# Performance work log

Hardware: AMD Instinct MI355X
Metric: run time of the kernel (lower is better)

Reference implementation:

```python
import jax, jax.numpy as jnp
import numpy as np

Q, B, N, DIM, HEADS, CODES = 4, 8, 4096, 1024, 8, 1024
DH = DIM // HEADS  # codebook_dim = 128
SCALE = DH ** -0.5


def setup_inputs() -> dict:
    key = jax.random.key(0)
    k0, k1, k2, k3 = jax.random.split(key, 4)
    return {
        "x": jax.random.normal(k0, (B, N, DIM), jnp.float32),
        "codes": jax.random.normal(k1, (Q, HEADS, CODES, DH), jnp.float32),
        "wk": jax.random.normal(k2, (Q, HEADS, DH, DH), jnp.float32) * SCALE,
        "wv": jax.random.normal(k3, (Q, HEADS, DH, DH), jnp.float32) * SCALE,
    }


def _memcodes_layer(x, codes, wk, wv):
    """One Memcodes quantizer (eval path: hard argmax).
    x: [B,N,DIM]; codes: [H,C,DH]; wk/wv: [H,DH,DH].
    Returns quantized [B,N,DIM], indices [B,H,N]."""
    b, n, _ = x.shape
    q = x.reshape(b, n, HEADS, DH).transpose(0, 2, 1, 3) * SCALE  # [b,h,n,d]
    k = jnp.einsum('hnd,hdc->hnc', codes, wk)  # [h,C,d]
    v = jnp.einsum('hnd,hdc->hnc', codes, wv)  # [h,C,d]
    logits = jnp.einsum('bhid,hjd->bhij', q, k)  # [b,h,n,C]
    idx = jnp.argmax(logits, axis=-1)  # [b,h,n]
    # one_hot(idx) @ v == gather rows of v at idx
    out = jnp.take_along_axis(v[None], idx[..., None], axis=2)  # [b,h,n,d]
    out = out.transpose(0, 2, 1, 3).reshape(b, n, DIM)
    return out, idx


def reference(x, codes, wk, wv):
    residual = x
    quantized_out = jnp.zeros_like(x)
    all_indices = []
    for i in range(Q):  # fixed small loop over quantizer layers
        quantized, idx = _memcodes_layer(residual, codes[i], wk[i], wv[i])
        residual = residual - quantized
        quantized_out = quantized_out + quantized
        all_indices.append(idx)
    return quantized_out, jnp.stack(all_indices, axis=-1)  # [B,N,DIM], [B,H,N,Q]
```

## Files before the change

kernel.cpp:

```cpp
#include <hip/hip_runtime.h>
#include <math.h>

#define QL 4
#define BB 8
#define NN 4096
#define DIMF 1024
#define HH 8
#define CC 1024
#define DH 128

#define MARGIN 4e-3f

typedef __attribute__((ext_vector_type(4))) float f32x4;
typedef __attribute__((ext_vector_type(8))) short s16x8;

__device__ __forceinline__ unsigned short f2bf(float f) {
    unsigned int u = __float_as_uint(f);
    u = u + 0x7fffu + ((u >> 16) & 1u);
    return (unsigned short)(u >> 16);
}
__device__ __forceinline__ float bf2f(unsigned short b) {
    return __uint_as_float(((unsigned int)b) << 16);
}
__device__ __forceinline__ void dma16(const void* g, void* l) {
    __builtin_amdgcn_global_load_lds(
        (const __attribute__((address_space(1))) unsigned int*)g,
        (__attribute__((address_space(3))) unsigned int*)l, 16, 0, 0);
}

#define MFMA(a, bb, c) c = __builtin_amdgcn_mfma_f32_16x16x32_bf16(a, bb, c, 0, 0, 0)

__device__ __forceinline__ void upd(float& m1, float& m2, int& mi, float v, int c) {
    if (v > m1) { m2 = m1; m1 = v; mi = c; }
    else if (v > m2) m2 = v;
}

__global__ __launch_bounds__(128) void kv_kernel(
    const float* __restrict__ codes, const float* __restrict__ wk,
    const float* __restrict__ wv, unsigned short* __restrict__ khi,
    unsigned short* __restrict__ klo, float* __restrict__ vbuf)
{
    __shared__ float sc[8][128];
    int bid = blockIdx.x;
    int cg  = bid & 127;
    int qh  = bid >> 7;
    int t   = threadIdx.x;

    const float* cbase = codes + ((size_t)qh * CC + (size_t)cg * 8) * DH;
    #pragma unroll
    for (int i = 0; i < 8; ++i) sc[i][t] = cbase[i * DH + t];
    __syncthreads();

    const float* wkb = wk + (size_t)qh * DH * DH;
    const float* wvb = wv + (size_t)qh * DH * DH;

    float ak[8], av[8];
    #pragma unroll
    for (int i = 0; i < 8; ++i) { ak[i] = 0.f; av[i] = 0.f; }

    for (int d = 0; d < DH; ++d) {
        float a = wkb[d * DH + t];
        float b = wvb[d * DH + t];
        #pragma unroll
        for (int i = 0; i < 8; ++i) {
            ak[i] = fmaf(sc[i][d], a, ak[i]);
            av[i] = fmaf(sc[i][d], b, av[i]);
        }
    }

    size_t base = ((size_t)qh * CC + (size_t)cg * 8) * DH + t;
    #pragma unroll
    for (int i = 0; i < 8; ++i) {
        float f = ak[i];
        unsigned short hb = f2bf(f);
        unsigned short lb = f2bf(f - bf2f(hb));
        khi[base + (size_t)i * DH]  = hb;
        klo[base + (size_t)i * DH]  = lb;
        vbuf[base + (size_t)i * DH] = av[i];
    }
}

__global__ __launch_bounds__(256, 2) void fused_kernel(
    const float* __restrict__ x, const unsigned short* __restrict__ khi,
    const unsigned short* __restrict__ klo, const float* __restrict__ vbuf,
    const float* __restrict__ codes, const float* __restrict__ wk,
    const float* __restrict__ wv, float* __restrict__ out)
{
    __shared__ __align__(16) char kstage[2][32768];
    __shared__ int    chosen[128];
    __shared__ float  smax1[128];
    __shared__ int    flagged[128];
    __shared__ int    hist[QL][128];
    __shared__ int    nflag;
    __shared__ float  rbuf32[DH];
    __shared__ double rbuf64[DH];
    __shared__ double pbuf[DH];
    __shared__ int    cand[64];
    __shared__ int    ncand;
    __shared__ int    bestc;
    __shared__ double bestv;

    const int t  = threadIdx.x;
    const int w  = t >> 6;
    const int l  = t & 63;
    const int lr = l & 15;
    const int lg = l >> 4;

    const int bid = blockIdx.x;
    const int h   = bid & 7;
    const int nt  = (bid >> 3) & 31;
    const int b   = bid >> 8;
    const int n0  = nt * 128;

    const int colE  = ((l & 15) << 4) ^ ((l >> 4) << 4) ^ (((l >> 3) & 1) << 5);
    const int loffE = ((l >> 4) << 8) + colE;
    const int loffO = loffE ^ 0x40;

    s16x8 rhi[2][4], rlo[2][4];
    #pragma unroll
    for (int s = 0; s < 2; ++s) {
        const int tok = (s * 4 + w) * 16 + lr;
        const float* xp = x + ((size_t)(b * NN + n0 + tok)) * DIMF + h * DH;
        #pragma unroll
        for (int ks = 0; ks < 4; ++ks) {
            const float* p = xp + ks * 32 + lg * 8;
            float4 a = *reinterpret_cast<const float4*>(p);
            float4 c = *reinterpret_cast<const float4*>(p + 4);
            float vv[8] = {a.x, a.y, a.z, a.w, c.x, c.y, c.z, c.w};
            s16x8 hi8, lo8;
            #pragma unroll
            for (int j = 0; j < 8; ++j) {
                unsigned short hb = f2bf(vv[j]);
                unsigned short lb = f2bf(vv[j] - bf2f(hb));
                hi8[j] = (short)hb; lo8[j] = (short)lb;
            }
            rhi[s][ks] = hi8; rlo[s][ks] = lo8;
        }
    }
    if (t == 0) nflag = 0;
    __syncthreads();

    for (int q = 0; q < QL; ++q) {
        const unsigned short* khq = khi + (size_t)(q * HH + h) * CC * DH;
        const unsigned short* klq = klo + (size_t)(q * HH + h) * CC * DH;
        const float* vq = vbuf + (size_t)(q * HH + h) * CC * DH;
        const char* khc = (const char*)khq;
        const char* klc = (const char*)klq;

        auto stage8 = [&](int buf, int chunk) {
            const char* gh = khc + chunk * 16384 + w * 4096;
            const char* gl = klc + chunk * 16384 + w * 4096;
            char* lb = &kstage[buf][0] + w * 4096;
            dma16(gh + loffE, lb);
            dma16(gh + 1024 + loffO, lb + 1024);
            dma16(gh + 2048 + loffE, lb + 2048);
            dma16(gh + 3072 + loffO, lb + 3072);
            dma16(gl + loffE, lb + 16384);
            dma16(gl + 1024 + loffO, lb + 16384 + 1024);
            dma16(gl + 2048 + loffE, lb + 16384 + 2048);
            dma16(gl + 3072 + loffO, lb + 16384 + 3072);
        };

        float bv[2][4], b2[2][4];
        int   bi[2][4];
        #pragma unroll
        for (int s = 0; s < 2; ++s)
            #pragma unroll
            for (int r = 0; r < 4; ++r) {
                bv[s][r] = -INFINITY; b2[s][r] = -INFINITY; bi[s][r] = 0;
            }

        stage8(0, 0);

        for (int ct = 0; ct < 16; ++ct) {
            const int cur = ct & 1;
            if (ct < 15) {
                stage8(cur ^ 1, ct + 1);
                asm volatile("s_waitcnt vmcnt(8)" ::: "memory");
            } else {
                asm volatile("s_waitcnt vmcnt(0)" ::: "memory");
            }
            __builtin_amdgcn_sched_barrier(0);
            __builtin_amdgcn_s_barrier();
            __builtin_amdgcn_sched_barrier(0);

            const char* Bb = &kstage[cur][0];
            f32x4 a00 = {0.f,0.f,0.f,0.f}, a01 = {0.f,0.f,0.f,0.f};
            f32x4 a02 = {0.f,0.f,0.f,0.f}, a03 = {0.f,0.f,0.f,0.f};
            f32x4 a10 = {0.f,0.f,0.f,0.f}, a11 = {0.f,0.f,0.f,0.f};
            f32x4 a12 = {0.f,0.f,0.f,0.f}, a13 = {0.f,0.f,0.f,0.f};

            #pragma unroll
            for (int ks = 0; ks < 4; ++ks) {
                const int swz = ((ks * 64 + lg * 16) ^ ((lr & 7) << 4)) ^ ((ks >> 1) << 5);
                const char* p0 = Bb + (lr)      * 256 + swz;
                const char* p1 = Bb + (16 + lr) * 256 + swz;
                const char* p2 = Bb + (32 + lr) * 256 + swz;
                const char* p3 = Bb + (48 + lr) * 256 + swz;
                s16x8 bh0 = *reinterpret_cast<const s16x8*>(p0);
                s16x8 bh1 = *reinterpret_cast<const s16x8*>(p1);
                s16x8 bh2 = *reinterpret_cast<const s16x8*>(p2);
                s16x8 bh3 = *reinterpret_cast<const s16x8*>(p3);
                s16x8 bl0 = *reinterpret_cast<const s16x8*>(p0 + 16384);
                s16x8 bl1 = *reinterpret_cast<const s16x8*>(p1 + 16384);
                s16x8 bl2 = *reinterpret_cast<const s16x8*>(p2 + 16384);
                s16x8 bl3 = *reinterpret_cast<const s16x8*>(p3 + 16384);

                __builtin_amdgcn_s_setprio(1);
                MFMA(rhi[0][ks], bh0, a00); MFMA(rhi[1][ks], bh0, a10);
                MFMA(rhi[0][ks], bh1, a01); MFMA(rhi[1][ks], bh1, a11);
                MFMA(rhi[0][ks], bh2, a02); MFMA(rhi[1][ks], bh2, a12);
                MFMA(rhi[0][ks], bh3, a03); MFMA(rhi[1][ks], bh3, a13);
                MFMA(rlo[0][ks], bh0, a00); MFMA(rlo[1][ks], bh0, a10);
                MFMA(rlo[0][ks], bh1, a01); MFMA(rlo[1][ks], bh1, a11);
                MFMA(rlo[0][ks], bh2, a02); MFMA(rlo[1][ks], bh2, a12);
                MFMA(rlo[0][ks], bh3, a03); MFMA(rlo[1][ks], bh3, a13);
                MFMA(rhi[0][ks], bl0, a00); MFMA(rhi[1][ks], bl0, a10);
                MFMA(rhi[0][ks], bl1, a01); MFMA(rhi[1][ks], bl1, a11);
                MFMA(rhi[0][ks], bl2, a02); MFMA(rhi[1][ks], bl2, a12);
                MFMA(rhi[0][ks], bl3, a03); MFMA(rhi[1][ks], bl3, a13);
                __builtin_amdgcn_s_setprio(0);
            }

            #pragma unroll
            for (int r = 0; r < 4; ++r) {
                const int cb = ct * 64 + lr;
                upd(bv[0][r], b2[0][r], bi[0][r], a00[r], cb);
                upd(bv[0][r], b2[0][r], bi[0][r], a01[r], cb + 16);
                upd(bv[0][r], b2[0][r], bi[0][r], a02[r], cb + 32);
                upd(bv[0][r], b2[0][r], bi[0][r], a03[r], cb + 48);
                upd(bv[1][r], b2[1][r], bi[1][r], a10[r], cb);
                upd(bv[1][r], b2[1][r], bi[1][r], a11[r], cb + 16);
                upd(bv[1][r], b2[1][r], bi[1][r], a12[r], cb + 32);
                upd(bv[1][r], b2[1][r], bi[1][r], a13[r], cb + 48);
            }

            __builtin_amdgcn_sched_barrier(0);
            __builtin_amdgcn_s_barrier();
            __builtin_amdgcn_sched_barrier(0);
        }

        #pragma unroll
        for (int s = 0; s < 2; ++s) {
            #pragma unroll
            for (int r = 0; r < 4; ++r) {
                float m = bv[s][r]; float m2 = b2[s][r]; int mi = bi[s][r];
                #pragma unroll
                for (int off = 1; off <= 8; off <<= 1) {
                    float ov = __shfl_xor(m, off);
                    int   oi = __shfl_xor(mi, off);
                    float o2 = __shfl_xor(m2, off);
                    float nm2 = fmaxf(fmaxf(m2, o2), fminf(m, ov));
                    if (ov > m || (ov == m && oi < mi)) { m = ov; mi = oi; }
                    m2 = nm2;
                }
                if (lr == 0) {
                    int tok = (s * 4 + w) * 16 + lg * 4 + r;
                    chosen[tok] = mi; smax1[tok] = m;
                    int fl = (m - m2 < MARGIN) ? 1 : 0;
                    flagged[tok] = fl;
                    if (fl) atomicAdd(&nflag, 1);
                }
            }
        }
        __syncthreads();

        int nf = nflag;
        if (nf) {
            for (int tok = 0; tok < 128; ++tok) {
                if (!flagged[tok]) continue;
                if (t == 0) { ncand = 0; bestc = 0x7fffffff; bestv = -1e300; }
                if (t < DH) {
                    double r = (double)x[((size_t)(b * NN + n0 + tok)) * DIMF + h * DH + t];
                    for (int qq = 0; qq < q; ++qq) {
                        int c = hist[qq][tok];
                        const float* crow = codes + ((size_t)(qq * HH + h) * CC + c) * DH;
                        const float* wcol = wv + (size_t)(qq * HH + h) * DH * DH + t;
                        double acc = 0.0;
                        for (int dd = 0; dd < DH; ++dd)
                            acc += (double)crow[dd] * (double)wcol[(size_t)dd * DH];
                        r -= acc;
                    }
                    rbuf64[t] = r;
                    rbuf32[t] = (float)r;
                }
                __syncthreads();
                float thr = smax1[tok] - MARGIN;
                #pragma unroll
                for (int cc4 = 0; cc4 < 4; ++cc4) {
                    int c = t * 4 + cc4;
                    const unsigned short* kh = khq + (size_t)c * DH;
                    const unsigned short* kl = klq + (size_t)c * DH;
                    float acc = 0.f;
                    for (int d = 0; d < DH; ++d)
                        acc = fmaf(bf2f(kh[d]) + bf2f(kl[d]), rbuf32[d], acc);
                    if (acc >= thr) {
                        int p = atomicAdd(&ncand, 1);
                        if (p < 64) cand[p] = c;
                    }
                }
                __syncthreads();
                int nc = ncand; if (nc > 64) nc = 64;
                for (int ci = 0; ci < nc; ++ci) {
                    int c = cand[ci];
                    if (t < DH) {
                        const float* crow = codes + ((size_t)(q * HH + h) * CC + c) * DH;
                        const float* wcol = wk + (size_t)(q * HH + h) * DH * DH + t;
                        double acc = 0.0;
                        for (int dd = 0; dd < DH; ++dd)
                            acc += (double)crow[dd] * (double)wcol[(size_t)dd * DH];
                        pbuf[t] = acc * rbuf64[t];
                    }
                    __syncthreads();
                    if (t == 0) {
                        double sm = 0.0;
                        for (int dd = 0; dd < DH; ++dd) sm += pbuf[dd];
                        if (sm > bestv || (sm == bestv && c < bestc)) { bestv = sm; bestc = c; }
                    }
                    __syncthreads();
                }
                if (t == 0) chosen[tok] = bestc;
                __syncthreads();
            }
        }

        if (t < 128) hist[q][t] = chosen[t];
        if (t == 0) nflag = 0;

        #pragma unroll
        for (int s = 0; s < 2; ++s) {
            const int tok = (s * 4 + w) * 16 + lr;
            const float* vrow = vq + (size_t)chosen[tok] * DH;
            #pragma unroll
            for (int ks = 0; ks < 4; ++ks) {
                const float* p = vrow + ks * 32 + lg * 8;
                float4 a = *reinterpret_cast<const float4*>(p);
                float4 c = *reinterpret_cast<const float4*>(p + 4);
                float vv[8] = {a.x, a.y, a.z, a.w, c.x, c.y, c.z, c.w};
                s16x8 hi8 = rhi[s][ks], lo8 = rlo[s][ks], nh, nl;
                #pragma unroll
                for (int j = 0; j < 8; ++j) {
                    float f = bf2f((unsigned short)hi8[j]) +
                              bf2f((unsigned short)lo8[j]) - vv[j];
                    unsigned short hb = f2bf(f);
                    nh[j] = (short)hb;
                    nl[j] = (short)f2bf(f - bf2f(hb));
                }
                rhi[s][ks] = nh; rlo[s][ks] = nl;
            }
        }
        __syncthreads();
    }

    #pragma unroll
    for (int s = 0; s < 2; ++s) {
        const int tok = (s * 4 + w) * 16 + lr;
        const float* xp = x + ((size_t)(b * NN + n0 + tok)) * DIMF + h * DH;
        float* op = out + ((size_t)(b * NN + n0 + tok)) * DIMF + h * DH;
        #pragma unroll
        for (int ks = 0; ks < 4; ++ks) {
            const float* p = xp + ks * 32 + lg * 8;
            float4 a = *reinterpret_cast<const float4*>(p);
            float4 c = *reinterpret_cast<const float4*>(p + 4);
            s16x8 hi8 = rhi[s][ks], lo8 = rlo[s][ks];
            float4 o0, o1;
            o0.x = a.x - (bf2f((unsigned short)hi8[0]) + bf2f((unsigned short)lo8[0]));
            o0.y = a.y - (bf2f((unsigned short)hi8[1]) + bf2f((unsigned short)lo8[1]));
            o0.z = a.z - (bf2f((unsigned short)hi8[2]) + bf2f((unsigned short)lo8[2]));
            o0.w = a.w - (bf2f((unsigned short)hi8[3]) + bf2f((unsigned short)lo8[3]));
            o1.x = c.x - (bf2f((unsigned short)hi8[4]) + bf2f((unsigned short)lo8[4]));
            o1.y = c.y - (bf2f((unsigned short)hi8[5]) + bf2f((unsigned short)lo8[5]));
            o1.z = c.z - (bf2f((unsigned short)hi8[6]) + bf2f((unsigned short)lo8[6]));
            o1.w = c.w - (bf2f((unsigned short)hi8[7]) + bf2f((unsigned short)lo8[7]));
            *reinterpret_cast<float4*>(op + ks * 32 + lg * 8)     = o0;
            *reinterpret_cast<float4*>(op + ks * 32 + lg * 8 + 4) = o1;
        }
    }

    __syncthreads();
    if (t < 128) {
        float4 iv;
        iv.x = (float)hist[0][t];
        iv.y = (float)hist[1][t];
        iv.z = (float)hist[2][t];
        iv.w = (float)hist[3][t];
        float* ip = out + (size_t)BB * NN * DIMF +
                    (((size_t)(b * HH + h) * NN) + n0 + t) * QL;
        *reinterpret_cast<float4*>(ip) = iv;
    }
}

extern "C" void kernel_launch(void* const* d_in, const int* in_sizes, int n_in,
                              void* d_out, int out_size, void* d_ws, size_t ws_size,
                              hipStream_t stream) {
    const float* x     = (const float*)d_in[0];
    const float* codes = (const float*)d_in[1];
    const float* wk    = (const float*)d_in[2];
    const float* wv    = (const float*)d_in[3];
    float* out  = (float*)d_out;

    float* vbuf = (float*)d_ws;
    unsigned short* khi = (unsigned short*)(vbuf + (size_t)QL * HH * CC * DH);
    unsigned short* klo = khi + (size_t)QL * HH * CC * DH;

    kv_kernel<<<QL * HH * CC / 8, 128, 0, stream>>>(codes, wk, wv, khi, klo, vbuf);
    fused_kernel<<<BB * HH * (NN / 128), 256, 0, stream>>>(x, khi, klo, vbuf,
                                                           codes, wk, wv, out);
}
```

Baseline: 1.202 ms.

## Double token tile per block to 256 and reuse each staged K fragment across four token groups

Each block now handles 256 tokens instead of 128, so every wave keeps four 16-token residual groups in registers. The inner loop is restructured to load one K hi/lo fragment per code tile and reuse it across all four token groups, which halves the number of blocks that stream the codebook through LDS. The running-max update is also rewritten with fmin/fmax to cut branching. The cost is roughly double the register use for residuals and argmax state, which may force spills or lower occupancy under launch_bounds(256,2), and there are half as many blocks to fill the GPU.

```diff
diff --git a/kernel.cpp b/kernel.cpp
--- a/kernel.cpp
+++ b/kernel.cpp
@@ -31,8 +31,8 @@
 #define MFMA(a, bb, c) c = __builtin_amdgcn_mfma_f32_16x16x32_bf16(a, bb, c, 0, 0, 0)
 
 __device__ __forceinline__ void upd(float& m1, float& m2, int& mi, float v, int c) {
-    if (v > m1) { m2 = m1; m1 = v; mi = c; }
-    else if (v > m2) m2 = v;
+    m2 = fmaxf(fminf(m1, v), m2);
+    if (v > m1) { m1 = v; mi = c; }
 }
 
 __global__ __launch_bounds__(128) void kv_kernel(
@@ -87,10 +87,10 @@
     const float* __restrict__ wv, float* __restrict__ out)
 {
     __shared__ __align__(16) char kstage[2][32768];
-    __shared__ int    chosen[128];
-    __shared__ float  smax1[128];
-    __shared__ int    flagged[128];
-    __shared__ int    hist[QL][128];
+    __shared__ int    chosen[256];
+    __shared__ float  smax1[256];
+    __shared__ int    flagged[256];
+    __shared__ int    hist[QL][256];
     __shared__ int    nflag;
     __shared__ float  rbuf32[DH];
     __shared__ double rbuf64[DH];
@@ -108,18 +108,18 @@
 
     const int bid = blockIdx.x;
     const int h   = bid & 7;
-    const int nt  = (bid >> 3) & 31;
-    const int b   = bid >> 8;
-    const int n0  = nt * 128;
+    const int nt  = (bid >> 3) & 15;
+    const int b   = bid >> 7;
+    const int n0  = nt * 256;
 
     const int colE  = ((l & 15) << 4) ^ ((l >> 4) << 4) ^ (((l >> 3) & 1) << 5);
     const int loffE = ((l >> 4) << 8) + colE;
     const int loffO = loffE ^ 0x40;
 
-    s16x8 rhi[2][4], rlo[2][4];
-    #pragma unroll
-    for (int s = 0; s < 2; ++s) {
-        const int tok = (s * 4 + w) * 16 + lr;
+    s16x8 rhi[4][4], rlo[4][4];
+    #pragma unroll
+    for (int s = 0; s < 4; ++s) {
+        const int tok = (w * 4 + s) * 16 + lr;
         const float* xp = x + ((size_t)(b * NN + n0 + tok)) * DIMF + h * DH;
         #pragma unroll
         for (int ks = 0; ks < 4; ++ks) {
@@ -161,10 +161,10 @@
             dma16(gl + 3072 + loffO, lb + 16384 + 3072);
         };
 
-        float bv[2][4], b2[2][4];
-        int   bi[2][4];
-        #pragma unroll
-        for (int s = 0; s < 2; ++s)
+        float bv[4][4], b2[4][4];
+        int   bi[4][4];
+        #pragma unroll
+        for (int s = 0; s < 4; ++s)
             #pragma unroll
             for (int r = 0; r < 4; ++r) {
                 bv[s][r] = -INFINITY; b2[s][r] = -INFINITY; bi[s][r] = 0;
@@ -185,54 +185,37 @@
             __builtin_amdgcn_sched_barrier(0);
 
             const char* Bb = &kstage[cur][0];
-            f32x4 a00 = {0.f,0.f,0.f,0.f}, a01 = {0.f,0.f,0.f,0.f};
-            f32x4 a02 = {0.f,0.f,0.f,0.f}, a03 = {0.f,0.f,0.f,0.f};
-            f32x4 a10 = {0.f,0.f,0.f,0.f}, a11 = {0.f,0.f,0.f,0.f};
-            f32x4 a12 = {0.f,0.f,0.f,0.f}, a13 = {0.f,0.f,0.f,0.f};
-
-            #pragma unroll
-            for (int ks = 0; ks < 4; ++ks) {
-                const int swz = ((ks * 64 + lg * 16) ^ ((lr & 7) << 4)) ^ ((ks >> 1) << 5);
-                const char* p0 = Bb + (lr)      * 256 + swz;
-                const char* p1 = Bb + (16 + lr) * 256 + swz;
-                const char* p2 = Bb + (32 + lr) * 256 + swz;
-                const char* p3 = Bb + (48 + lr) * 256 + swz;
-                s16x8 bh0 = *reinterpret_cast<const s16x8*>(p0);
-                s16x8 bh1 = *reinterpret_cast<const s16x8*>(p1);
-                s16x8 bh2 = *reinterpret_cast<const s16x8*>(p2);
-                s16x8 bh3 = *reinterpret_cast<const s16x8*>(p3);
-                s16x8 bl0 = *reinterpret_cast<const s16x8*>(p0 + 16384);
-                s16x8 bl1 = *reinterpret_cast<const s16x8*>(p1 + 16384);
-                s16x8 bl2 = *reinterpret_cast<const s16x8*>(p2 + 16384);
-                s16x8 bl3 = *reinterpret_cast<const s16x8*>(p3 + 16384);
-
-                __builtin_amdgcn_s_setprio(1);
-                MFMA(rhi[0][ks], bh0, a00); MFMA(rhi[1][ks], bh0, a10);
-                MFMA(rhi[0][ks], bh1, a01); MFMA(rhi[1][ks], bh1, a11);
-                MFMA(rhi[0][ks], bh2, a02); MFMA(rhi[1][ks], bh2, a12);
-                MFMA(rhi[0][ks], bh3, a03); MFMA(rhi[1][ks], bh3, a13);
-                MFMA(rlo[0][ks], bh0, a00); MFMA(rlo[1][ks], bh0, a10);
-                MFMA(rlo[0][ks], bh1, a01); MFMA(rlo[1][ks], bh1, a11);
-                MFMA(rlo[0][ks], bh2, a02); MFMA(rlo[1][ks], bh2, a12);
-                MFMA(rlo[0][ks], bh3, a03); MFMA(rlo[1][ks], bh3, a13);
-                MFMA(rhi[0][ks], bl0, a00); MFMA(rhi[1][ks], bl0, a10);
-                MFMA(rhi[0][ks], bl1, a01); MFMA(rhi[1][ks], bl1, a11);
-                MFMA(rhi[0][ks], bl2, a02); MFMA(rhi[1][ks], bl2, a12);
-                MFMA(rhi[0][ks], bl3, a03); MFMA(rhi[1][ks], bl3, a13);
-                __builtin_amdgcn_s_setprio(0);
-            }
-
-            #pragma unroll
-            for (int r = 0; r < 4; ++r) {
-                const int cb = ct * 64 + lr;
-                upd(bv[0][r], b2[0][r], bi[0][r], a00[r], cb);
-                upd(bv[0][r], b2[0][r], bi[0][r], a01[r], cb + 16);
-                upd(bv[0][r], b2[0][r], bi[0][r], a02[r], cb + 32);
-                upd(bv[0][r], b2[0][r], bi[0][r], a03[r], cb + 48);
-                upd(bv[1][r], b2[1][r], bi[1][r], a10[r], cb);
-                upd(bv[1][r], b2[1][r], bi[1][r], a11[r], cb + 16);
-                upd(bv[1][r], b2[1][r], bi[1][r], a12[r], cb + 32);
-                upd(bv[1][r], b2[1][r], bi[1][r], a13[r], cb + 48);
+
+            #pragma unroll
+            for (int ctile = 0; ctile < 4; ++ctile) {
+                f32x4 a0 = {0.f,0.f,0.f,0.f}, a1 = {0.f,0.f,0.f,0.f};
+                f32x4 a2 = {0.f,0.f,0.f,0.f}, a3 = {0.f,0.f,0.f,0.f};
+
+                #pragma unroll
+                for (int ks = 0; ks < 4; ++ks) {
+                    const int swz = ((ks * 64 + lg * 16) ^ ((lr & 7) << 4)) ^ ((ks >> 1) << 5);
+                    const char* p = Bb + (ctile * 16 + lr) * 256 + swz;
+                    s16x8 bh = *reinterpret_cast<const s16x8*>(p);
+                    s16x8 bl = *reinterpret_cast<const s16x8*>(p + 16384);
+
+                    __builtin_amdgcn_s_setprio(1);
+                    MFMA(rhi[0][ks], bh, a0); MFMA(rhi[1][ks], bh, a1);
+                    MFMA(rhi[2][ks], bh, a2); MFMA(rhi[3][ks], bh, a3);
+                    MFMA(rlo[0][ks], bh, a0); MFMA(rlo[1][ks], bh, a1);
+                    MFMA(rlo[2][ks], bh, a2); MFMA(rlo[3][ks], bh, a3);
+                    MFMA(rhi[0][ks], bl, a0); MFMA(rhi[1][ks], bl, a1);
+                    MFMA(rhi[2][ks], bl, a2); MFMA(rhi[3][ks], bl, a3);
+                    __builtin_amdgcn_s_setprio(0);
+                }
+
+                const int cb = ct * 64 + ctile * 16 + lr;
+                #pragma unroll
+                for (int r = 0; r < 4; ++r) {
+                    upd(bv[0][r], b2[0][r], bi[0][r], a0[r], cb);
+                    upd(bv[1][r], b2[1][r], bi[1][r], a1[r], cb);
+                    upd(bv[2][r], b2[2][r], bi[2][r], a2[r], cb);
+                    upd(bv[3][r], b2[3][r], bi[3][r], a3[r], cb);
+                }
             }
 
             __builtin_amdgcn_sched_barrier(0);
@@ -241,7 +224,7 @@
         }
 
         #pragma unroll
-        for (int s = 0; s < 2; ++s) {
+        for (int s = 0; s < 4; ++s) {
             #pragma unroll
             for (int r = 0; r < 4; ++r) {
                 float m = bv[s][r]; float m2 = b2[s][r]; int mi = bi[s][r];
@@ -255,7 +238,7 @@
                     m2 = nm2;
                 }
                 if (lr == 0) {
-                    int tok = (s * 4 + w) * 16 + lg * 4 + r;
+                    int tok = (w * 4 + s) * 16 + lg * 4 + r;
                     chosen[tok] = mi; smax1[tok] = m;
                     int fl = (m - m2 < MARGIN) ? 1 : 0;
                     flagged[tok] = fl;
@@ -267,7 +250,7 @@
 
         int nf = nflag;
         if (nf) {
-            for (int tok = 0; tok < 128; ++tok) {
+            for (int tok = 0; tok < 256; ++tok) {
                 if (!flagged[tok]) continue;
                 if (t == 0) { ncand = 0; bestc = 0x7fffffff; bestv = -1e300; }
                 if (t < DH) {
@@ -324,12 +307,12 @@
             }
         }
 
-        if (t < 128) hist[q][t] = chosen[t];
+        hist[q][t] = chosen[t];
         if (t == 0) nflag = 0;
 
         #pragma unroll
-        for (int s = 0; s < 2; ++s) {
-            const int tok = (s * 4 + w) * 16 + lr;
+        for (int s = 0; s < 4; ++s) {
+            const int tok = (w * 4 + s) * 16 + lr;
             const float* vrow = vq + (size_t)chosen[tok] * DH;
             #pragma unroll
             for (int ks = 0; ks < 4; ++ks) {
@@ -353,8 +336,8 @@
     }
 
     #pragma unroll
-    for (int s = 0; s < 2; ++s) {
-        const int tok = (s * 4 + w) * 16 + lr;
+    for (int s = 0; s < 4; ++s) {
+        const int tok = (w * 4 + s) * 16 + lr;
         const float* xp = x + ((size_t)(b * NN + n0 + tok)) * DIMF + h * DH;
         float* op = out + ((size_t)(b * NN + n0 + tok)) * DIMF + h * DH;
         #pragma unroll
@@ -378,7 +361,7 @@
     }
 
     __syncthreads();
-    if (t < 128) {
+    {
         float4 iv;
         iv.x = (float)hist[0][t];
         iv.y = (float)hist[1][t];
@@ -404,6 +387,6 @@
     unsigned short* klo = khi + (size_t)QL * HH * CC * DH;
 
     kv_kernel<<<QL * HH * CC / 8, 128, 0, stream>>>(codes, wk, wv, khi, klo, vbuf);
-    fused_kernel<<<BB * HH * (NN / 128), 256, 0, stream>>>(x, khi, klo, vbuf,
+    fused_kernel<<<BB * HH * (NN / 256), 256, 0, stream>>>(x, khi, klo, vbuf,
                                                            codes, wk, wv, out);
 }
```

Result: slower. 1.352 ms (+12.5%).

## Halve code tile per stage to cut LDS and raise occupancy to three blocks

Applied to the files above, without the earlier changes.

The per-iteration code tile shrinks from 64 to 32 codes. This halves the double-buffered LDS staging (64KB to 32KB) and the accumulator registers, and launch bounds now ask for 3 blocks per CU. The running top-2 update is also made branch-light with fmin/fmax. The trade-off is twice as many loop iterations and barriers, with less MFMA work between each sync.

```diff
diff --git a/kernel.cpp b/kernel.cpp
--- a/kernel.cpp
+++ b/kernel.cpp
@@ -31,8 +31,8 @@
 #define MFMA(a, bb, c) c = __builtin_amdgcn_mfma_f32_16x16x32_bf16(a, bb, c, 0, 0, 0)
 
 __device__ __forceinline__ void upd(float& m1, float& m2, int& mi, float v, int c) {
-    if (v > m1) { m2 = m1; m1 = v; mi = c; }
-    else if (v > m2) m2 = v;
+    m2 = fmaxf(fminf(m1, v), m2);
+    if (v > m1) { m1 = v; mi = c; }
 }
 
 __global__ __launch_bounds__(128) void kv_kernel(
@@ -80,13 +80,13 @@
     }
 }
 
-__global__ __launch_bounds__(256, 2) void fused_kernel(
+__global__ __launch_bounds__(256, 3) void fused_kernel(
     const float* __restrict__ x, const unsigned short* __restrict__ khi,
     const unsigned short* __restrict__ klo, const float* __restrict__ vbuf,
     const float* __restrict__ codes, const float* __restrict__ wk,
     const float* __restrict__ wv, float* __restrict__ out)
 {
-    __shared__ __align__(16) char kstage[2][32768];
+    __shared__ __align__(16) char kstage[2][16384];
     __shared__ int    chosen[128];
     __shared__ float  smax1[128];
     __shared__ int    flagged[128];
@@ -147,18 +147,14 @@
         const char* khc = (const char*)khq;
         const char* klc = (const char*)klq;
 
-        auto stage8 = [&](int buf, int chunk) {
-            const char* gh = khc + chunk * 16384 + w * 4096;
-            const char* gl = klc + chunk * 16384 + w * 4096;
-            char* lb = &kstage[buf][0] + w * 4096;
+        auto stage4 = [&](int buf, int chunk) {
+            const char* gh = khc + chunk * 8192 + w * 2048;
+            const char* gl = klc + chunk * 8192 + w * 2048;
+            char* lb = &kstage[buf][0] + w * 2048;
             dma16(gh + loffE, lb);
             dma16(gh + 1024 + loffO, lb + 1024);
-            dma16(gh + 2048 + loffE, lb + 2048);
-            dma16(gh + 3072 + loffO, lb + 3072);
-            dma16(gl + loffE, lb + 16384);
-            dma16(gl + 1024 + loffO, lb + 16384 + 1024);
-            dma16(gl + 2048 + loffE, lb + 16384 + 2048);
-            dma16(gl + 3072 + loffO, lb + 16384 + 3072);
+            dma16(gl + loffE, lb + 8192);
+            dma16(gl + 1024 + loffO, lb + 8192 + 1024);
         };
 
         float bv[2][4], b2[2][4];
@@ -170,13 +166,13 @@
                 bv[s][r] = -INFINITY; b2[s][r] = -INFINITY; bi[s][r] = 0;
             }
 
-        stage8(0, 0);
-
-        for (int ct = 0; ct < 16; ++ct) {
+        stage4(0, 0);
+
+        for (int ct = 0; ct < 32; ++ct) {
             const int cur = ct & 1;
-            if (ct < 15) {
-                stage8(cur ^ 1, ct + 1);
-                asm volatile("s_waitcnt vmcnt(8)" ::: "memory");
+            if (ct < 31) {
+                stage4(cur ^ 1, ct + 1);
+                asm volatile("s_waitcnt vmcnt(4)" ::: "memory");
             } else {
                 asm volatile("s_waitcnt vmcnt(0)" ::: "memory");
             }
@@ -186,53 +182,37 @@
 
             const char* Bb = &kstage[cur][0];
             f32x4 a00 = {0.f,0.f,0.f,0.f}, a01 = {0.f,0.f,0.f,0.f};
-            f32x4 a02 = {0.f,0.f,0.f,0.f}, a03 = {0.f,0.f,0.f,0.f};
             f32x4 a10 = {0.f,0.f,0.f,0.f}, a11 = {0.f,0.f,0.f,0.f};
-            f32x4 a12 = {0.f,0.f,0.f,0.f}, a13 = {0.f,0.f,0.f,0.f};
 
             #pragma unroll
             for (int ks = 0; ks < 4; ++ks) {
                 const int swz = ((ks * 64 + lg * 16) ^ ((lr & 7) << 4)) ^ ((ks >> 1) << 5);
                 const char* p0 = Bb + (lr)      * 256 + swz;
                 const char* p1 = Bb + (16 + lr) * 256 + swz;
-                const char* p2 = Bb + (32 + lr) * 256 + swz;
-                const char* p3 = Bb + (48 + lr) * 256 + swz;
                 s16x8 bh0 = *reinterpret_cast<const s16x8*>(p0);
                 s16x8 bh1 = *reinterpret_cast<const s16x8*>(p1);
-                s16x8 bh2 = *reinterpret_cast<const s16x8*>(p2);
-                s16x8 bh3 = *reinterpret_cast<const s16x8*>(p3);
-                s16x8 bl0 = *reinterpret_cast<const s16x8*>(p0 + 16384);
-                s16x8 bl1 = *reinterpret_cast<const s16x8*>(p1 + 16384);
-                s16x8 bl2 = *reinterpret_cast<const s16x8*>(p2 + 16384);
-                s16x8 bl3 = *reinterpret_cast<const s16x8*>(p3 + 16384);
+                s16x8 bl0 = *reinterpret_cast<const s16x8*>(p0 + 8192);
+                s16x8 bl1 = *reinterpret_cast<const s16x8*>(p1 + 8192);
 
                 __builtin_amdgcn_s_setprio(1);
                 MFMA(rhi[0][ks], bh0, a00); MFMA(rhi[1][ks], bh0, a10);
                 MFMA(rhi[0][ks], bh1, a01); MFMA(rhi[1][ks], bh1, a11);
-                MFMA(rhi[0][ks], bh2, a02); MFMA(rhi[1][ks], bh2, a12);
-                MFMA(rhi[0][ks], bh3, a03); MFMA(rhi[1][ks], bh3, a13);
                 MFMA(rlo[0][ks], bh0, a00); MFMA(rlo[1][ks], bh0, a10);
                 MFMA(rlo[0][ks], bh1, a01); MFMA(rlo[1][ks], bh1, a11);
-                MFMA(rlo[0][ks], bh2, a02); MFMA(rlo[1][ks], bh2, a12);
-                MFMA(rlo[0][ks], bh3, a03); MFMA(rlo[1][ks], bh3, a13);
                 MFMA(rhi[0][ks], bl0, a00); MFMA(rhi[1][ks], bl0, a10);
                 MFMA(rhi[0][ks], bl1, a01); MFMA(rhi[1][ks], bl1, a11);
-                MFMA(rhi[0][ks], bl2, a02); MFMA(rhi[1][ks], bl2, a12);
-                MFMA(rhi[0][ks], bl3, a03); MFMA(rhi[1][ks], bl3, a13);
                 __builtin_amdgcn_s_setprio(0);
             }
 
-            #pragma unroll
-            for (int r = 0; r < 4; ++r) {
-                const int cb = ct * 64 + lr;
-                upd(bv[0][r], b2[0][r], bi[0][r], a00[r], cb);
-                upd(bv[0][r], b2[0][r], bi[0][r], a01[r], cb + 16);
-                upd(bv[0][r], b2[0][r], bi[0][r], a02[r], cb + 32);
-                upd(bv[0][r], b2[0][r], bi[0][r], a03[r], cb + 48);
-                upd(bv[1][r], b2[1][r], bi[1][r], a10[r], cb);
-                upd(bv[1][r], b2[1][r], bi[1][r], a11[r], cb + 16);
-                upd(bv[1][r], b2[1][r], bi[1][r], a12[r], cb + 32);
-                upd(bv[1][r], b2[1][r], bi[1][r], a13[r], cb + 48);
+            {
+                const int cb = ct * 32 + lr;
+                #pragma unroll
+                for (int r = 0; r < 4; ++r) {
+                    upd(bv[0][r], b2[0][r], bi[0][r], a00[r], cb);
+                    upd(bv[0][r], b2[0][r], bi[0][r], a01[r], cb + 16);
+                    upd(bv[1][r], b2[1][r], bi[1][r], a10[r], cb);
+                    upd(bv[1][r], b2[1][r], bi[1][r], a11[r], cb + 16);
+                }
             }
 
             __builtin_amdgcn_sched_barrier(0);
```

After: 1.087 ms. -9.6%, faster.
